# Kernel tuning notes

Hardware: AMD Instinct MI355X
Metric: run time of the kernel (lower is better)

## Reference

```python
import jax, jax.numpy as jnp
import numpy as np

N_NODES = 50000
N_EDGES = 800000
D_IN = 128
D_OUT = 128


def setup_inputs() -> dict:
    key = jax.random.key(0)
    k1, k2, k3, k4, k5, k6 = jax.random.split(key, 6)
    x = jax.random.normal(k1, (N_NODES, D_IN), dtype=jnp.float32)
    edge_row = jnp.sort(jax.random.randint(k2, (N_EDGES,), 0, N_NODES, dtype=jnp.int32))
    edge_col = jax.random.randint(k3, (N_EDGES,), 0, N_NODES, dtype=jnp.int32)
    edge_val = jax.random.uniform(k4, (N_EDGES,), dtype=jnp.float32)
    W = jax.random.uniform(k5, (D_OUT, D_IN), dtype=jnp.float32)  # torch Linear weight [out,in], uniform_ init
    b = jax.random.normal(k6, (D_OUT,), dtype=jnp.float32)
    return {"x": x, "edge_row": edge_row, "edge_col": edge_col,
            "edge_val": edge_val, "W": W, "b": b}


def reference(x, edge_row, edge_col, edge_val, W, b):
    # spmm: out[i] = sum_{e: row[e]==i} val[e] * x[col[e]]
    msgs = x[edge_col] * edge_val[:, None]            # [E, D_IN]
    agg = jax.ops.segment_sum(msgs, edge_row, num_segments=x.shape[0])  # [N, D_IN]
    # dropout is identity in eval mode; linear projection y = agg @ W^T + b
    return agg @ W.T + b
```

## Files before the change

### kernel.cpp

```cpp
#include <hip/hip_runtime.h>
#include <hip/hip_bf16.h>


#define NPB     16
#define NPP     64
#define BLOCK   256
#define D       128
#define CHUNK   512
#define ASTRIDE 136

typedef __attribute__((ext_vector_type(8))) short bf16x8;
typedef __attribute__((ext_vector_type(4))) float f32x4;
typedef __attribute__((ext_vector_type(2))) float v2f;

__device__ __forceinline__ short f2bf(float f) {
    unsigned u = __float_as_uint(f);
    unsigned r = (u + 0x7fffu + ((u >> 16) & 1u)) >> 16;
    return (short)r;
}
__device__ __forceinline__ float bf_lo(int w) { return __int_as_float(w << 16); }
__device__ __forceinline__ float bf_hi(int w) { return __int_as_float(w & 0xffff0000); }

__global__ __launch_bounds__(256, 4)
void prepass_kernel(const float* __restrict__ x,
                    const float* __restrict__ W,
                    const int*   __restrict__ edge_row,
                    short* __restrict__ yb,
                    int*   __restrict__ rs,
                    int n_nodes, int n_edges, int gemm_blocks)
{
    const int bid = blockIdx.x;
    const int tid = threadIdx.x;

    if (bid >= gemm_blocks) {
        const int gid = (bid - gemm_blocks) * 256 + tid;
        if (gid <= n_nodes) {
            int lo = 0, hi = n_edges;
            while (lo < hi) {
                int mid = (lo + hi) >> 1;
                bool lt = (edge_row[mid] < gid);
                lo = lt ? (mid + 1) : lo;
                hi = lt ? hi : mid;
            }
            rs[gid] = lo;
        }
        return;
    }

    __shared__ __align__(16) short xa_s[NPP * ASTRIDE];

    const int wave = tid >> 6;
    const int lane = tid & 63;
    const int tile_base = bid * NPP;

    #pragma unroll
    for (int t = 0; t < 8; ++t) {
        int idx = t * 256 + tid;
        int row = idx >> 5;
        int c4  = idx & 31;
        int node = tile_base + row;
        float4 v = (node < n_nodes)
            ? reinterpret_cast<const float4*>(x)[(size_t)node * 32 + c4]
            : make_float4(0.f, 0.f, 0.f, 0.f);
        *reinterpret_cast<short4*>(&xa_s[row * ASTRIDE + c4 * 4]) =
            make_short4(f2bf(v.x), f2bf(v.y), f2bf(v.z), f2bf(v.w));
    }

    const int n16 = lane & 15;
    const int g   = lane >> 4;

    bf16x8 bfr[2][4];
    #pragma unroll
    for (int tt = 0; tt < 2; ++tt) {
        const int jt = 2 * wave + tt;
        const float* wrow = W + (size_t)(jt * 16 + n16) * D + g * 8;
        #pragma unroll
        for (int ks = 0; ks < 4; ++ks) {
            float4 wa  = *reinterpret_cast<const float4*>(wrow + ks * 32);
            float4 wb4 = *reinterpret_cast<const float4*>(wrow + ks * 32 + 4);
            bf16x8 f;
            f[0] = f2bf(wa.x);  f[1] = f2bf(wa.y);  f[2] = f2bf(wa.z);  f[3] = f2bf(wa.w);
            f[4] = f2bf(wb4.x); f[5] = f2bf(wb4.y); f[6] = f2bf(wb4.z); f[7] = f2bf(wb4.w);
            bfr[tt][ks] = f;
        }
    }

    __syncthreads();

    #pragma unroll
    for (int st = 0; st < 4; ++st) {
        const int rbase = st * 16;
        bf16x8 afr[4];
        #pragma unroll
        for (int ks = 0; ks < 4; ++ks)
            afr[ks] = *reinterpret_cast<const bf16x8*>(
                &xa_s[(rbase + n16) * ASTRIDE + ks * 32 + g * 8]);

        #pragma unroll
        for (int tt = 0; tt < 2; ++tt) {
            const int jt = 2 * wave + tt;
            const int j  = jt * 16 + n16;
            f32x4 c = {0.f, 0.f, 0.f, 0.f};
            #pragma unroll
            for (int ks = 0; ks < 4; ++ks)
                c = __builtin_amdgcn_mfma_f32_16x16x32_bf16(afr[ks], bfr[tt][ks], c, 0, 0, 0);
            #pragma unroll
            for (int r = 0; r < 4; ++r) {
                int node = tile_base + rbase + g * 4 + r;
                if (node < n_nodes)
                    yb[(size_t)node * D + j] = f2bf(c[r]);
            }
        }
    }
}

__global__ __launch_bounds__(BLOCK, 6)
void gcn_main_kernel(const short* __restrict__ yb,
                     const int*   __restrict__ rs_g,
                     const int*   __restrict__ edge_col,
                     const float* __restrict__ edge_val,
                     const float* __restrict__ bvec,
                     float*       __restrict__ out,
                     int n_nodes, int n_edges)
{
    __shared__ int2 cv_s[CHUNK];
    __shared__ int  rs_s[NPB + 1];

    const int tid  = threadIdx.x;
    const int wave = tid >> 6;
    const int lane = tid & 63;
    const int tile_base = blockIdx.x * NPB;

    if (tid <= NPB) rs_s[tid] = rs_g[min(tile_base + tid, n_nodes)];
    __syncthreads();

    const int E0 = __builtin_amdgcn_readfirstlane(rs_s[0]);
    const int E1 = __builtin_amdgcn_readfirstlane(rs_s[NPB]);
    const int cnt = min(E1 - E0, CHUNK);

    for (int i = tid; i < cnt; i += BLOCK)
        cv_s[i] = make_int2(edge_col[E0 + i], __float_as_int(edge_val[E0 + i]));
    __syncthreads();

    const int p = lane >> 4;
    const int q = lane & 15;
    const int n = wave * 4 + p;
    const int e0 = rs_s[n], e1 = rs_s[n + 1];
    const int cap  = E0 + cnt;
    const int ecap = min(e1, cap);
    const short* yq = yb + q * 8;

    v2f acc2[4];
    #pragma unroll
    for (int i = 0; i < 4; ++i) acc2[i] = (v2f){0.f, 0.f};

    for (int e = e0; e < ecap; e += 8) {
        int2 cv[8];
        int4 xr[8];
        #pragma unroll
        for (int u = 0; u < 8; ++u) {
            int idx = e + u;
            int il  = (idx < ecap) ? (idx - E0) : (e0 - E0);
            cv[u] = cv_s[il];
        }
        #pragma unroll
        for (int u = 0; u < 8; ++u)
            xr[u] = *reinterpret_cast<const int4*>(yq + ((size_t)cv[u].x << 7));
        #pragma unroll
        for (int u = 0; u < 8; ++u) {
            float vm = (e + u < ecap) ? __int_as_float(cv[u].y) : 0.f;
            v2f v2 = (v2f){vm, vm};
            acc2[0] += v2 * (v2f){bf_lo(xr[u].x), bf_hi(xr[u].x)};
            acc2[1] += v2 * (v2f){bf_lo(xr[u].y), bf_hi(xr[u].y)};
            acc2[2] += v2 * (v2f){bf_lo(xr[u].z), bf_hi(xr[u].z)};
            acc2[3] += v2 * (v2f){bf_lo(xr[u].w), bf_hi(xr[u].w)};
        }
    }
    for (int e = max(e0, cap); e < e1; ++e) {
        int   c = edge_col[e];
        float v = edge_val[e];
        int4 xr = *reinterpret_cast<const int4*>(yq + ((size_t)c << 7));
        v2f v2 = (v2f){v, v};
        acc2[0] += v2 * (v2f){bf_lo(xr.x), bf_hi(xr.x)};
        acc2[1] += v2 * (v2f){bf_lo(xr.y), bf_hi(xr.y)};
        acc2[2] += v2 * (v2f){bf_lo(xr.z), bf_hi(xr.z)};
        acc2[3] += v2 * (v2f){bf_lo(xr.w), bf_hi(xr.w)};
    }

    const int node = tile_base + n;
    if (node < n_nodes) {
        const float* bq = bvec + q * 8;
        float4 b0 = *reinterpret_cast<const float4*>(bq);
        float4 b1 = *reinterpret_cast<const float4*>(bq + 4);
        float* orow = out + (size_t)node * D + q * 8;
        float4 o0 = make_float4(acc2[0].x + b0.x, acc2[0].y + b0.y,
                                acc2[1].x + b0.z, acc2[1].y + b0.w);
        float4 o1 = make_float4(acc2[2].x + b1.x, acc2[2].y + b1.y,
                                acc2[3].x + b1.z, acc2[3].y + b1.w);
        *reinterpret_cast<float4*>(orow)     = o0;
        *reinterpret_cast<float4*>(orow + 4) = o1;
    }
}

__global__ __launch_bounds__(BLOCK, 5)
void gcn_fallback_kernel(const float* __restrict__ x,
                         const int*   __restrict__ edge_row,
                         const int*   __restrict__ edge_col,
                         const float* __restrict__ edge_val,
                         const float* __restrict__ W,
                         const float* __restrict__ bvec,
                         float*       __restrict__ out,
                         int n_nodes, int n_edges)
{
    __shared__ __align__(16) short agg_s[NPB * ASTRIDE];
    __shared__ int rs_s[NPB + 1];

    const int tid  = threadIdx.x;
    const int wave = tid >> 6;
    const int lane = tid & 63;
    const int tile_base = blockIdx.x * NPB;

    if (tid <= NPB) {
        int target = tile_base + tid;
        if (target > n_nodes) target = n_nodes;
        int lo = 0, hi = n_edges;
        while (lo < hi) {
            int mid = (lo + hi) >> 1;
            lo = (edge_row[mid] < target) ? (mid + 1) : lo;
            hi = (edge_row[mid] < target) ? hi : mid;
        }
        rs_s[tid] = lo;
    }
    __syncthreads();

    {
        const int h = lane >> 5;
        const int q = lane & 31;
        const float* xq = x + (q << 2);

        #pragma unroll
        for (int ni = 0; ni < NPB / 4; ++ni) {
            const int n = wave + 4 * ni;
            const int e0 = __builtin_amdgcn_readfirstlane(rs_s[n]);
            const int e1 = __builtin_amdgcn_readfirstlane(rs_s[n + 1]);
            float ax = 0.f, ay = 0.f, az = 0.f, aw = 0.f;
            for (int e = e0; e < e1; e += 16) {
                #pragma unroll
                for (int u = 0; u < 8; ++u) {
                    int idx  = e + 2 * u + h;
                    int idxc = (idx < e1) ? idx : (e1 - 1);
                    int   c  = edge_col[idxc];
                    float vr = edge_val[idxc];
                    float v  = (idx < e1) ? vr : 0.f;
                    float4 xr = *reinterpret_cast<const float4*>(xq + ((size_t)c << 7));
                    ax += v * xr.x; ay += v * xr.y; az += v * xr.z; aw += v * xr.w;
                }
            }
            ax += __shfl_xor(ax, 32, 64); ay += __shfl_xor(ay, 32, 64);
            az += __shfl_xor(az, 32, 64); aw += __shfl_xor(aw, 32, 64);
            if (h == 0) {
                *reinterpret_cast<short4*>(&agg_s[n * ASTRIDE + (q << 2)]) =
                    make_short4(f2bf(ax), f2bf(ay), f2bf(az), f2bf(aw));
            }
        }
    }

    const int n16 = lane & 15;
    const int g   = lane >> 4;
    bf16x8 bfr[2][4];
    #pragma unroll
    for (int tt = 0; tt < 2; ++tt) {
        const int jt = 2 * wave + tt;
        const float* rowp = W + ((size_t)(jt * 16 + n16)) * D + g * 8;
        #pragma unroll
        for (int ks = 0; ks < 4; ++ks) {
            float4 wa  = *reinterpret_cast<const float4*>(rowp + ks * 32);
            float4 wb4 = *reinterpret_cast<const float4*>(rowp + ks * 32 + 4);
            bf16x8 f;
            f[0] = f2bf(wa.x);  f[1] = f2bf(wa.y);  f[2] = f2bf(wa.z);  f[3] = f2bf(wa.w);
            f[4] = f2bf(wb4.x); f[5] = f2bf(wb4.y); f[6] = f2bf(wb4.z); f[7] = f2bf(wb4.w);
            bfr[tt][ks] = f;
        }
    }
    __syncthreads();
    {
        bf16x8 afr[4];
        #pragma unroll
        for (int ks = 0; ks < 4; ++ks)
            afr[ks] = *reinterpret_cast<const bf16x8*>(&agg_s[n16 * ASTRIDE + ks * 32 + g * 8]);
        #pragma unroll
        for (int tt = 0; tt < 2; ++tt) {
            const int jt = 2 * wave + tt;
            const int j  = jt * 16 + n16;
            const float bj = bvec[j];
            f32x4 c = {0.f, 0.f, 0.f, 0.f};
            #pragma unroll
            for (int ks = 0; ks < 4; ++ks)
                c = __builtin_amdgcn_mfma_f32_16x16x32_bf16(afr[ks], bfr[tt][ks], c, 0, 0, 0);
            #pragma unroll
            for (int r = 0; r < 4; ++r) {
                int node = tile_base + g * 4 + r;
                if (node < n_nodes)
                    out[(size_t)node * D + j] = c[r] + bj;
            }
        }
    }
}

extern "C" void kernel_launch(void* const* d_in, const int* in_sizes, int n_in,
                              void* d_out, int out_size, void* d_ws, size_t ws_size,
                              hipStream_t stream) {
    const float* x        = (const float*)d_in[0];
    const int*   edge_row = (const int*)  d_in[1];
    const int*   edge_col = (const int*)  d_in[2];
    const float* edge_val = (const float*)d_in[3];
    const float* W        = (const float*)d_in[4];
    const float* b        = (const float*)d_in[5];
    float* out = (float*)d_out;

    const int n_nodes = in_sizes[0] / D;
    const int n_edges = in_sizes[1];
    const int grid = (n_nodes + NPB - 1) / NPB;

    const size_t yb_bytes = (size_t)n_nodes * D * sizeof(short);
    const size_t rs_bytes = (size_t)(n_nodes + 1) * sizeof(int);
    if (ws_size >= yb_bytes + rs_bytes) {
        short* yb = (short*)d_ws;
        int*   rs = (int*)((char*)d_ws + yb_bytes);
        const int gemm_blocks   = (n_nodes + NPP - 1) / NPP;
        const int search_blocks = (n_nodes + 1 + 255) / 256;
        prepass_kernel<<<gemm_blocks + search_blocks, 256, 0, stream>>>(
            x, W, edge_row, yb, rs, n_nodes, n_edges, gemm_blocks);
        gcn_main_kernel<<<grid, BLOCK, 0, stream>>>(yb, rs, edge_col, edge_val,
                                                    b, out, n_nodes, n_edges);
    } else {
        gcn_fallback_kernel<<<grid, BLOCK, 0, stream>>>(x, edge_row, edge_col, edge_val,
                                                        W, b, out, n_nodes, n_edges);
    }
}
```

Before: 125.0 us.

## Split projected features into column planes and gather in four passes

The prepass writes the bf16 projected features into four column planes of 32 columns each instead of one row-major matrix. The aggregation kernel is launched once per plane and gathers 4 bytes per lane per edge, writing a 32-column slice of the output. The aim is for each plane's working set to fit in cache during the random gathers. In exchange, the edge list and row offsets are re-read four times, there are more launches, and each gather access is narrower.

New measurement: 142.6 us. 1.14x slower.

```diff
diff --git a/kernel.cpp b/kernel.cpp
--- a/kernel.cpp
+++ b/kernel.cpp
@@ -8,6 +8,7 @@
 #define D       128
 #define CHUNK   512
 #define ASTRIDE 136
+#define PCOLS   32
 
 typedef __attribute__((ext_vector_type(8))) short bf16x8;
 typedef __attribute__((ext_vector_type(4))) float f32x4;
@@ -99,7 +100,9 @@
         #pragma unroll
         for (int tt = 0; tt < 2; ++tt) {
             const int jt = 2 * wave + tt;
-            const int j  = jt * 16 + n16;
+            const int p  = jt >> 1;
+            const int c0 = (jt & 1) * 16 + n16;
+            short* pl = yb + (size_t)p * n_nodes * PCOLS;
             f32x4 c = {0.f, 0.f, 0.f, 0.f};
             #pragma unroll
             for (int ks = 0; ks < 4; ++ks)
@@ -108,20 +111,20 @@
             for (int r = 0; r < 4; ++r) {
                 int node = tile_base + rbase + g * 4 + r;
                 if (node < n_nodes)
-                    yb[(size_t)node * D + j] = f2bf(c[r]);
-            }
-        }
-    }
-}
-
-__global__ __launch_bounds__(BLOCK, 6)
-void gcn_main_kernel(const short* __restrict__ yb,
+                    pl[(size_t)node * PCOLS + c0] = f2bf(c[r]);
+            }
+        }
+    }
+}
+
+__global__ __launch_bounds__(BLOCK, 7)
+void gcn_pass_kernel(const short* __restrict__ plane,
                      const int*   __restrict__ rs_g,
                      const int*   __restrict__ edge_col,
                      const float* __restrict__ edge_val,
                      const float* __restrict__ bvec,
                      float*       __restrict__ out,
-                     int n_nodes, int n_edges)
+                     int n_nodes, int n_edges, int pass)
 {
     __shared__ int2 cv_s[CHUNK];
     __shared__ int  rs_s[NPB + 1];
@@ -142,21 +145,19 @@
         cv_s[i] = make_int2(edge_col[E0 + i], __float_as_int(edge_val[E0 + i]));
     __syncthreads();
 
-    const int p = lane >> 4;
-    const int q = lane & 15;
-    const int n = wave * 4 + p;
+    const int pq = lane >> 4;
+    const int q  = lane & 15;
+    const int n  = wave * 4 + pq;
     const int e0 = rs_s[n], e1 = rs_s[n + 1];
     const int cap  = E0 + cnt;
     const int ecap = min(e1, cap);
-    const short* yq = yb + q * 8;
-
-    v2f acc2[4];
-    #pragma unroll
-    for (int i = 0; i < 4; ++i) acc2[i] = (v2f){0.f, 0.f};
+    const short* yq = plane + q * 2;
+
+    v2f acc = (v2f){0.f, 0.f};
 
     for (int e = e0; e < ecap; e += 8) {
         int2 cv[8];
-        int4 xr[8];
+        int  xr[8];
         #pragma unroll
         for (int u = 0; u < 8; ++u) {
             int idx = e + u;
@@ -165,40 +166,26 @@
         }
         #pragma unroll
         for (int u = 0; u < 8; ++u)
-            xr[u] = *reinterpret_cast<const int4*>(yq + ((size_t)cv[u].x << 7));
+            xr[u] = *reinterpret_cast<const int*>(yq + ((size_t)cv[u].x << 5));
         #pragma unroll
         for (int u = 0; u < 8; ++u) {
             float vm = (e + u < ecap) ? __int_as_float(cv[u].y) : 0.f;
-            v2f v2 = (v2f){vm, vm};
-            acc2[0] += v2 * (v2f){bf_lo(xr[u].x), bf_hi(xr[u].x)};
-            acc2[1] += v2 * (v2f){bf_lo(xr[u].y), bf_hi(xr[u].y)};
-            acc2[2] += v2 * (v2f){bf_lo(xr[u].z), bf_hi(xr[u].z)};
-            acc2[3] += v2 * (v2f){bf_lo(xr[u].w), bf_hi(xr[u].w)};
+            acc += (v2f){vm, vm} * (v2f){bf_lo(xr[u]), bf_hi(xr[u])};
         }
     }
     for (int e = max(e0, cap); e < e1; ++e) {
         int   c = edge_col[e];
         float v = edge_val[e];
-        int4 xr = *reinterpret_cast<const int4*>(yq + ((size_t)c << 7));
-        v2f v2 = (v2f){v, v};
-        acc2[0] += v2 * (v2f){bf_lo(xr.x), bf_hi(xr.x)};
-        acc2[1] += v2 * (v2f){bf_lo(xr.y), bf_hi(xr.y)};
-        acc2[2] += v2 * (v2f){bf_lo(xr.z), bf_hi(xr.z)};
-        acc2[3] += v2 * (v2f){bf_lo(xr.w), bf_hi(xr.w)};
+        int  xr = *reinterpret_cast<const int*>(yq + ((size_t)c << 5));
+        acc += (v2f){v, v} * (v2f){bf_lo(xr), bf_hi(xr)};
     }
 
     const int node = tile_base + n;
     if (node < n_nodes) {
-        const float* bq = bvec + q * 8;
-        float4 b0 = *reinterpret_cast<const float4*>(bq);
-        float4 b1 = *reinterpret_cast<const float4*>(bq + 4);
-        float* orow = out + (size_t)node * D + q * 8;
-        float4 o0 = make_float4(acc2[0].x + b0.x, acc2[0].y + b0.y,
-                                acc2[1].x + b0.z, acc2[1].y + b0.w);
-        float4 o1 = make_float4(acc2[2].x + b1.x, acc2[2].y + b1.y,
-                                acc2[3].x + b1.z, acc2[3].y + b1.w);
-        *reinterpret_cast<float4*>(orow)     = o0;
-        *reinterpret_cast<float4*>(orow + 4) = o1;
+        const int cbase = pass * PCOLS + q * 2;
+        float2 bb = *reinterpret_cast<const float2*>(bvec + cbase);
+        float2 o  = make_float2(acc.x + bb.x, acc.y + bb.y);
+        *reinterpret_cast<float2*>(out + (size_t)node * D + cbase) = o;
     }
 }
 
@@ -331,8 +318,11 @@
         const int search_blocks = (n_nodes + 1 + 255) / 256;
         prepass_kernel<<<gemm_blocks + search_blocks, 256, 0, stream>>>(
             x, W, edge_row, yb, rs, n_nodes, n_edges, gemm_blocks);
-        gcn_main_kernel<<<grid, BLOCK, 0, stream>>>(yb, rs, edge_col, edge_val,
-                                                    b, out, n_nodes, n_edges);
+        for (int p = 0; p < 4; ++p) {
+            const short* plane = yb + (size_t)p * n_nodes * PCOLS;
+            gcn_pass_kernel<<<grid, BLOCK, 0, stream>>>(plane, rs, edge_col, edge_val,
+                                                        b, out, n_nodes, n_edges, p);
+        }
     } else {
         gcn_fallback_kernel<<<grid, BLOCK, 0, stream>>>(x, edge_row, edge_col, edge_val,
                                                         W, b, out, n_nodes, n_edges);
```
